# Kernel optimization log

Hardware: AMD Instinct MI355X
Metric: run time of the kernel (lower is better)

The kernel has to match this reference:

```python
import jax, jax.numpy as jnp
import numpy as np

B, C, INNER, H, W = 32, 256, 128, 32, 32
EPS = 1e-5


def _conv1x1(x, w):
    # x: (B, Cin, H, W); w: (Cout, Cin) -> (B, Cout, H, W)
    return jnp.einsum('bchw,oc->bohw', x, w)


def _attend(q, k, v):
    # q,k: (B, D, H, W); v: (B, C, H, W)
    b, d, h, w = q.shape
    n = h * w
    qf = q.reshape(b, d, n).transpose(0, 2, 1)            # (B, N, D)
    kf = k.reshape(b, d, n).transpose(0, 2, 1)            # (B, N, D)
    vf = v.reshape(b, v.shape[1], n).transpose(0, 2, 1)   # (B, N, C)
    scale = 1.0 / jnp.sqrt(jnp.asarray(d, qf.dtype))
    attn = jax.nn.softmax(jnp.einsum('bnd,bmd->bnm', qf, kf) * scale, axis=-1)
    of = jnp.einsum('bnm,bmc->bnc', attn, vf)             # (B, N, C)
    return of.transpose(0, 2, 1).reshape(b, -1, h, w)


def _layernorm(x, w, b):
    # Normalize over (C, H, W) jointly; affine params broadcast from (C,1,1).
    mu = jnp.mean(x, axis=(1, 2, 3), keepdims=True)
    var = jnp.mean(jnp.square(x - mu), axis=(1, 2, 3), keepdims=True)
    return (x - mu) * jax.lax.rsqrt(var + EPS) * w[None] + b[None]


def setup_inputs() -> dict:
    key = jax.random.key(0)
    ks = jax.random.split(key, 10)
    s = 0.02
    return {
        'fs': jax.random.normal(ks[0], (B, C, H, W), jnp.float32),
        'fi': jax.random.normal(ks[1], (B, C, H, W), jnp.float32),
        'qs_w': jax.random.normal(ks[2], (INNER, C), jnp.float32) * s,
        'ks_w': jax.random.normal(ks[3], (INNER, C), jnp.float32) * s,
        'vs_w': jax.random.normal(ks[4], (C, C), jnp.float32) * s,
        'qi_w': jax.random.normal(ks[5], (INNER, C), jnp.float32) * s,
        'ki_w': jax.random.normal(ks[6], (INNER, C), jnp.float32) * s,
        'vi_w': jax.random.normal(ks[7], (C, C), jnp.float32) * s,
        'fuse_w': jax.random.normal(ks[8], (C, 2 * C), jnp.float32) * s,
        'fuse_b': jnp.zeros((C,), jnp.float32),
        'ln_s_w': jnp.ones((C, 1, 1), jnp.float32),
        'ln_s_b': jnp.zeros((C, 1, 1), jnp.float32),
        'ln_i_w': jnp.ones((C, 1, 1), jnp.float32),
        'ln_i_b': jnp.zeros((C, 1, 1), jnp.float32),
    }


def reference(fs, fi, qs_w, ks_w, vs_w, qi_w, ki_w, vi_w,
              fuse_w, fuse_b, ln_s_w, ln_s_b, ln_i_w, ln_i_b):
    # sketch queries attend over image keys/values
    s2i = _attend(_conv1x1(fs, qs_w), _conv1x1(fi, ki_w), _conv1x1(fi, vi_w))
    # image queries attend over sketch keys/values
    i2s = _attend(_conv1x1(fi, qi_w), _conv1x1(fs, ks_w), _conv1x1(fs, vs_w))

    def fuse(x):
        return jax.nn.relu(_conv1x1(x, fuse_w) + fuse_b[None, :, None, None])

    fs_out = _layernorm(fuse(jnp.concatenate([fs, i2s], axis=1)) + fs, ln_s_w, ln_s_b)
    fi_out = _layernorm(fuse(jnp.concatenate([fi, s2i], axis=1)) + fi, ln_i_w, ln_i_b)
    return (fs_out, fi_out)
```

## Files before the change

### kernel.cpp

```cpp
#include <hip/hip_runtime.h>

typedef unsigned short u16;
typedef unsigned int   u32;

#define B_   32
#define C_   256
#define N_   1024
#define CN_  (C_*N_)
#define EPS_ 1e-5f

typedef __attribute__((ext_vector_type(8))) short  short8;
typedef __attribute__((ext_vector_type(4))) float  f32x4;

__device__ __forceinline__ float b2f(u16 u){
  union { u32 u; float f; } c; c.u = ((u32)u) << 16; return c.f;
}
__device__ __forceinline__ u16 f2b(float f){
  union { float f; u32 u; } c; c.f = f;
  u32 u = c.u;
  return (u16)((u + 0x7FFFu + ((u >> 16) & 1u)) >> 16);
}

struct F4v { float v[4]; };

__device__ __forceinline__ F4v ld4g(const void* p, long i, int bf){
  F4v r;
  if (bf){
    ushort4 u = *(const ushort4*)((const u16*)p + i);
    r.v[0]=b2f(u.x); r.v[1]=b2f(u.y); r.v[2]=b2f(u.z); r.v[3]=b2f(u.w);
  } else {
    float4 f = *(const float4*)((const float*)p + i);
    r.v[0]=f.x; r.v[1]=f.y; r.v[2]=f.z; r.v[3]=f.w;
  }
  return r;
}
__device__ __forceinline__ float ld1g(const void* p, long i, int bf){
  return bf ? b2f(((const u16*)p)[i]) : ((const float*)p)[i];
}
__device__ __forceinline__ void st1g(void* p, long i, float v, int bf){
  if (bf) ((u16*)p)[i] = f2b(v); else ((float*)p)[i] = v;
}
__device__ __forceinline__ void st4g(void* p, long i, const float* v, int bf){
  if (bf){
    ushort4 u;
    u.x=f2b(v[0]); u.y=f2b(v[1]); u.z=f2b(v[2]); u.w=f2b(v[3]);
    *(ushort4*)((u16*)p + i) = u;
  } else {
    *(float4*)((float*)p + i) = make_float4(v[0],v[1],v[2],v[3]);
  }
}
__device__ __forceinline__ int sniff_bf(const void* lnw){
  return (*(const u32*)lnw == 0x3F803F80u) ? 1 : 0;
}

__global__ __launch_bounds__(256) void k_prep_w(
    const void* qs, const void* ks, const void* vs,
    const void* qi, const void* ki, const void* vi,
    const void* fw, const void* lnw,
    u16* __restrict__ Wcat, u16* __restrict__ fuseWb, float* __restrict__ stats)
{
  const int bf = sniff_bf(lnw);
  if (blockIdx.x == 0 && threadIdx.x < 128) stats[threadIdx.x] = 0.0f;
  const long idx = ((long)blockIdx.x*256 + threadIdx.x) * 4;
  if (idx < 262144){
    const int side = (int)(idx >> 17);
    const int rem  = (int)(idx & 131071);
    const int row  = rem >> 8, col = rem & 255;
    const void* src; int r2;
    if (row < 128)      { src = side ? qi : qs; r2 = row; }
    else if (row < 256) { src = side ? ki : ks; r2 = row - 128; }
    else                { src = side ? vi : vs; r2 = row - 256; }
    F4v v = ld4g(src, (long)r2*256 + col, bf);
    ushort4 u; u.x=f2b(v.v[0]); u.y=f2b(v.v[1]); u.z=f2b(v.v[2]); u.w=f2b(v.v[3]);
    *(ushort4*)&Wcat[idx] = u;
  } else {
    const long j = idx - 262144;
    F4v v = ld4g(fw, j, bf);
    ushort4 u; u.x=f2b(v.v[0]); u.y=f2b(v.v[1]); u.z=f2b(v.v[2]); u.w=f2b(v.v[3]);
    *(ushort4*)&fuseWb[j] = u;
  }
}

__global__ __launch_bounds__(256) void k_prep_t(
    const void* fs, const void* fi, const void* lnw, u16* __restrict__ Ft)
{
  const int bf = sniff_bf(lnw);
  const int nt = blockIdx.x, ct = blockIdx.y, bs = blockIdx.z;
  const int b = bs >> 1, side = bs & 1;
  const void* F = side ? fi : fs;
  const int t = threadIdx.x;
  __shared__ u16 T[64][72];
  const int c0 = ct << 6, n0 = nt << 6;
  const int nc = (t & 15) << 2, cl = t >> 4;
  #pragma unroll
  for (int p = 0; p < 4; p++){
    const int c = cl + (p << 4);
    F4v v = ld4g(F, ((long)b*C_ + c0 + c)*N_ + n0 + nc, bf);
    T[nc  ][c] = f2b(v.v[0]);
    T[nc+1][c] = f2b(v.v[1]);
    T[nc+2][c] = f2b(v.v[2]);
    T[nc+3][c] = f2b(v.v[3]);
  }
  __syncthreads();
  const int nl = t >> 2, cc = (t & 3) << 4;
  float4 x0 = *(const float4*)&T[nl][cc];
  float4 x1 = *(const float4*)&T[nl][cc + 8];
  u16* dst = Ft + ((long)bs << 18) + (long)(n0 + nl)*256 + c0 + cc;
  *(float4*)dst = x0;
  *(float4*)(dst + 8) = x1;
}

__global__ __launch_bounds__(256) void k_proj(
    const u16* __restrict__ Wcat, const u16* __restrict__ Ft,
    u16* __restrict__ QKp, u16* __restrict__ Vp)
{
  const int nt = blockIdx.x;
  const int ot = blockIdx.y;
  const int bs = blockIdx.z;
  const int side = bs & 1;
  const int t = threadIdx.x;
  const int wv = t >> 6, li = t & 15, qd = (t >> 4) & 3;
  const int o0 = (ot << 7) + (wv << 5);
  const int n0 = nt << 7;

  const u16* ap = Wcat + ((long)side*512 + o0 + li)*256 + qd*8;
  const u16* bp = Ft + ((long)bs << 18) + (long)(n0 + li)*256 + qd*8;

  const f32x4 z4 = {0.f,0.f,0.f,0.f};
  f32x4 acc[2][8];
  #pragma unroll
  for (int i = 0; i < 2; i++)
    #pragma unroll
    for (int j = 0; j < 8; j++) acc[i][j] = z4;

  for (int ks = 0; ks < 8; ks++){
    const int ko = ks*32;
    short8 a0 = *(const short8*)(ap + ko);
    short8 a1 = *(const short8*)(ap + 16*256 + ko);
    short8 bfr[8];
    #pragma unroll
    for (int j = 0; j < 8; j++) bfr[j] = *(const short8*)(bp + (long)j*16*256 + ko);
    #pragma unroll
    for (int j = 0; j < 8; j++){
      acc[0][j] = __builtin_amdgcn_mfma_f32_16x16x32_bf16(a0, bfr[j], acc[0][j], 0, 0, 0);
      acc[1][j] = __builtin_amdgcn_mfma_f32_16x16x32_bf16(a1, bfr[j], acc[1][j], 0, 0, 0);
    }
  }

  if (o0 < 256){
    u16* base = QKp + ((long)bs << 18);
    #pragma unroll
    for (int mi = 0; mi < 2; mi++){
      const int ocol = o0 + mi*16 + qd*4;
      #pragma unroll
      for (int j = 0; j < 8; j++){
        const int n = n0 + j*16 + li;
        ushort4 u;
        u.x = f2b(acc[mi][j][0]); u.y = f2b(acc[mi][j][1]);
        u.z = f2b(acc[mi][j][2]); u.w = f2b(acc[mi][j][3]);
        *(ushort4*)&base[(long)n*256 + ocol] = u;
      }
    }
  } else {
    u16* base = Vp + ((long)bs << 18);
    #pragma unroll
    for (int mi = 0; mi < 2; mi++){
      #pragma unroll
      for (int j = 0; j < 8; j++){
        const int n = n0 + j*16 + li;
        #pragma unroll
        for (int r = 0; r < 4; r++){
          const int c = o0 - 256 + mi*16 + qd*4 + r;
          base[(long)c*N_ + n] = f2b(acc[mi][j][r]);
        }
      }
    }
  }
}

__global__ __launch_bounds__(256) void k_attn(
    const u16* __restrict__ QKp, const u16* __restrict__ Vp, u16* __restrict__ AOt)
{
  const int nt = blockIdx.x;
  const int tt = blockIdx.y;
  const int b  = blockIdx.z;
  const int qside = 1 - tt, kvside = tt;
  const u16* Qb = QKp + (((long)(b*2+qside)) << 18);
  const u16* Kb = QKp + (((long)(b*2+kvside)) << 18) + 128;
  const u16* Vb = Vp  + (((long)(b*2+kvside)) << 18);

  const int t  = threadIdx.x;
  const int wv = t >> 6;
  const int li = t & 15;
  const int qd = (t >> 4) & 3;
  const int n0 = nt << 6;
  const int qb = wv << 4;
  const int cb = wv << 6;

  __shared__ __align__(16) u16 Pt[64][72];
  __shared__ float alphaS[64];
  __shared__ float lS[64];

  short8 qf[4];
  {
    const u16* qrow = Qb + (long)(n0 + qb + li)*256 + qd*8;
    #pragma unroll
    for (int kk = 0; kk < 4; kk++) qf[kk] = *(const short8*)(qrow + kk*32);
  }

  const f32x4 z4 = {0.f, 0.f, 0.f, 0.f};
  f32x4 accO[4][4];
  #pragma unroll
  for (int i = 0; i < 4; i++)
    #pragma unroll
    for (int j = 0; j < 4; j++) accO[i][j] = z4;
  float mst[4], lst[4];
  #pragma unroll
  for (int r = 0; r < 4; r++){ mst[r] = -1e30f; lst[r] = 0.0f; }
  const float scale = 0.088388347648318447f;

  for (int mt = 0; mt < 16; mt++){
    const int m0 = mt << 6;
    f32x4 sf[4];
    #pragma unroll
    for (int j = 0; j < 4; j++) sf[j] = z4;
    {
      const u16* krow = Kb + (long)(m0 + li)*256 + qd*8;
      #pragma unroll
      for (int j4 = 0; j4 < 4; j4++){
        #pragma unroll
        for (int kk = 0; kk < 4; kk++){
          short8 kf = *(const short8*)(krow + (long)j4*16*256 + kk*32);
          sf[j4] = __builtin_amdgcn_mfma_f32_16x16x32_bf16(qf[kk], kf, sf[j4], 0, 0, 0);
        }
      }
    }
    float al4[4];
    #pragma unroll
    for (int r = 0; r < 4; r++){
      float v0 = sf[0][r]*scale, v1 = sf[1][r]*scale;
      float v2 = sf[2][r]*scale, v3 = sf[3][r]*scale;
      float mx = fmaxf(fmaxf(v0,v1), fmaxf(v2,v3));
      mx = fmaxf(mx, __shfl_xor(mx, 1, 64));
      mx = fmaxf(mx, __shfl_xor(mx, 2, 64));
      mx = fmaxf(mx, __shfl_xor(mx, 4, 64));
      mx = fmaxf(mx, __shfl_xor(mx, 8, 64));
      float mn = fmaxf(mst[r], mx);
      float a  = __expf(mst[r] - mn);
      float p0 = __expf(v0 - mn), p1 = __expf(v1 - mn);
      float p2 = __expf(v2 - mn), p3 = __expf(v3 - mn);
      const int q = qb + (qd<<2) + r;
      Pt[q][     li] = f2b(p0);
      Pt[q][16 + li] = f2b(p1);
      Pt[q][32 + li] = f2b(p2);
      Pt[q][48 + li] = f2b(p3);
      float sm = p0 + p1 + p2 + p3;
      sm += __shfl_xor(sm, 1, 64);
      sm += __shfl_xor(sm, 2, 64);
      sm += __shfl_xor(sm, 4, 64);
      sm += __shfl_xor(sm, 8, 64);
      lst[r] = lst[r]*a + sm;
      mst[r] = mn;
      al4[r] = a;
    }
    if (li == 0){
      #pragma unroll
      for (int r = 0; r < 4; r++) alphaS[qb + (qd<<2) + r] = al4[r];
    }
    __syncthreads();
    {
      float aq[4];
      #pragma unroll
      for (int j4 = 0; j4 < 4; j4++) aq[j4] = alphaS[(j4<<4) + li];
      #pragma unroll
      for (int i4 = 0; i4 < 4; i4++)
        #pragma unroll
        for (int j4 = 0; j4 < 4; j4++){
          accO[i4][j4][0] *= aq[j4]; accO[i4][j4][1] *= aq[j4];
          accO[i4][j4][2] *= aq[j4]; accO[i4][j4][3] *= aq[j4];
        }
      short8 va[4][2];
      const u16* vrow = Vb + (long)(cb + li)*N_ + m0 + qd*8;
      #pragma unroll
      for (int i4 = 0; i4 < 4; i4++){
        va[i4][0] = *(const short8*)(vrow + (long)i4*16*N_);
        va[i4][1] = *(const short8*)(vrow + (long)i4*16*N_ + 32);
      }
      #pragma unroll
      for (int j4 = 0; j4 < 4; j4++){
        short8 pb0 = *(const short8*)&Pt[(j4<<4) + li][qd*8];
        short8 pb1 = *(const short8*)&Pt[(j4<<4) + li][qd*8 + 32];
        #pragma unroll
        for (int i4 = 0; i4 < 4; i4++){
          accO[i4][j4] = __builtin_amdgcn_mfma_f32_16x16x32_bf16(va[i4][0], pb0, accO[i4][j4], 0, 0, 0);
          accO[i4][j4] = __builtin_amdgcn_mfma_f32_16x16x32_bf16(va[i4][1], pb1, accO[i4][j4], 0, 0, 0);
        }
      }
    }
    __syncthreads();
  }
  if (li == 0){
    #pragma unroll
    for (int r = 0; r < 4; r++) lS[qb + (qd<<2) + r] = lst[r];
  }
  __syncthreads();
  float linv[4];
  #pragma unroll
  for (int j4 = 0; j4 < 4; j4++) linv[j4] = 1.0f / lS[(j4<<4) + li];
  u16* aob = AOt + (((long)(b*2+tt)) << 18);
  #pragma unroll
  for (int i4 = 0; i4 < 4; i4++){
    #pragma unroll
    for (int j4 = 0; j4 < 4; j4++){
      const int n = n0 + (j4<<4) + li;
      ushort4 u;
      u.x = f2b(accO[i4][j4][0] * linv[j4]);
      u.y = f2b(accO[i4][j4][1] * linv[j4]);
      u.z = f2b(accO[i4][j4][2] * linv[j4]);
      u.w = f2b(accO[i4][j4][3] * linv[j4]);
      *(ushort4*)&aob[(long)n*256 + cb + (i4<<4) + (qd<<2)] = u;
    }
  }
}

__global__ __launch_bounds__(256) void k_fuse(
    const void* fs, const void* fi, const u16* __restrict__ fuseWb,
    const void* fbias, const u16* __restrict__ Ft, const u16* __restrict__ AOt,
    void* out, float* __restrict__ stats, const void* lnw)
{
  const int bf = sniff_bf(lnw);
  const int nt = blockIdx.x;
  const int ot = blockIdx.y;
  const int bw = blockIdx.z;
  const int b = bw >> 1, w = bw & 1;
  const void* F = w ? fi : fs;
  const int t = threadIdx.x;
  const int wv = t >> 6, li = t & 15, qd = (t >> 4) & 3;
  const int o0 = (ot << 7) + (wv << 5);
  const int n0 = nt << 7;

  const u16* ap  = fuseWb + (long)(o0 + li)*512 + qd*8;
  const u16* bp1 = Ft  + ((long)bw << 18) + (long)(n0 + li)*256 + qd*8;
  const u16* bp2 = AOt + ((long)bw << 18) + (long)(n0 + li)*256 + qd*8;

  const f32x4 z4 = {0.f,0.f,0.f,0.f};
  f32x4 acc[2][8];
  #pragma unroll
  for (int i = 0; i < 2; i++)
    #pragma unroll
    for (int j = 0; j < 8; j++) acc[i][j] = z4;

  for (int ks = 0; ks < 16; ks++){
    const u16* bp = (ks < 8) ? (bp1 + ks*32) : (bp2 + (ks-8)*32);
    const int ko = ks*32;
    short8 a0 = *(const short8*)(ap + ko);
    short8 a1 = *(const short8*)(ap + 16*512 + ko);
    short8 bfr[8];
    #pragma unroll
    for (int j = 0; j < 8; j++) bfr[j] = *(const short8*)(bp + (long)j*16*256);
    #pragma unroll
    for (int j = 0; j < 8; j++){
      acc[0][j] = __builtin_amdgcn_mfma_f32_16x16x32_bf16(a0, bfr[j], acc[0][j], 0, 0, 0);
      acc[1][j] = __builtin_amdgcn_mfma_f32_16x16x32_bf16(a1, bfr[j], acc[1][j], 0, 0, 0);
    }
  }

  __shared__ float rbuf[8];
  float s1 = 0.0f, s2 = 0.0f;
  #pragma unroll
  for (int mi = 0; mi < 2; mi++){
    float biasv[4];
    #pragma unroll
    for (int r = 0; r < 4; r++) biasv[r] = ld1g(fbias, o0 + mi*16 + qd*4 + r, bf);
    #pragma unroll
    for (int j = 0; j < 8; j++){
      const int n = n0 + j*16 + li;
      #pragma unroll
      for (int r = 0; r < 4; r++){
        const int o = o0 + mi*16 + qd*4 + r;
        const float res = ld1g(F, ((long)b*C_ + o)*N_ + n, bf);
        float y = acc[mi][j][r] + biasv[r];
        y = y > 0.0f ? y : 0.0f;
        y += res;
        s1 += y; s2 += y*y;
        st1g(out, ((long)w*B_ + b)*CN_ + (long)o*N_ + n, y, bf);
      }
    }
  }
  #pragma unroll
  for (int off = 32; off > 0; off >>= 1){
    s1 += __shfl_down(s1, off, 64);
    s2 += __shfl_down(s2, off, 64);
  }
  const int lane = t & 63;
  if (lane == 0){ rbuf[wv*2] = s1; rbuf[wv*2+1] = s2; }
  __syncthreads();
  if (t == 0){
    atomicAdd(&stats[bw*2  ], rbuf[0]+rbuf[2]+rbuf[4]+rbuf[6]);
    atomicAdd(&stats[bw*2+1], rbuf[1]+rbuf[3]+rbuf[5]+rbuf[7]);
  }
}

__global__ __launch_bounds__(256) void k_ln(
    void* out, const float* __restrict__ stats,
    const void* lsw, const void* lsb, const void* liw, const void* lib)
{
  const int bf = sniff_bf(lsw);
  const long g = ((long)blockIdx.x*256 + threadIdx.x) * 4;
  const long half = (long)B_*CN_;
  const int w = (g >= half) ? 1 : 0;
  const long rem = g - (long)w*half;
  const int b  = (int)(rem >> 18);
  const int cn = (int)(rem & (CN_-1));
  const int c  = cn >> 10;
  const float s1v = stats[(b*2+w)*2], s2v = stats[(b*2+w)*2+1];
  const float inv = 1.0f / (float)CN_;
  const float mean = s1v * inv;
  const float var  = s2v * inv - mean*mean;
  const float rstd = rsqrtf(var + EPS_);
  const float lw = ld1g(w ? liw : lsw, c, bf);
  const float lb = ld1g(w ? lib : lsb, c, bf);
  F4v x = ld4g(out, g, bf);
  float vv[4];
  #pragma unroll
  for (int j = 0; j < 4; j++) vv[j] = (x.v[j] - mean)*rstd*lw + lb;
  st4g(out, g, vv, bf);
}

extern "C" void kernel_launch(void* const* d_in, const int* in_sizes, int n_in,
                              void* d_out, int out_size, void* d_ws, size_t ws_size,
                              hipStream_t stream)
{
  const void* fs     = d_in[0];
  const void* fi     = d_in[1];
  const void* qs_w   = d_in[2];
  const void* ks_w   = d_in[3];
  const void* vs_w   = d_in[4];
  const void* qi_w   = d_in[5];
  const void* ki_w   = d_in[6];
  const void* vi_w   = d_in[7];
  const void* fuse_w = d_in[8];
  const void* fuse_b = d_in[9];
  const void* ln_s_w = d_in[10];
  const void* ln_s_b = d_in[11];
  const void* ln_i_w = d_in[12];
  const void* ln_i_b = d_in[13];

  char* ws = (char*)d_ws;
  float* stats  = (float*)ws;
  u16*   Wcat   = (u16*)(ws + 4096);
  u16*   fuseWb = (u16*)(ws + 4096 + 524288);
  u16*   Ft     = (u16*)(ws + (1u<<20));
  u16*   QKp    = (u16*)(ws + (1u<<20) + (1u<<25));
  u16*   Vp     = (u16*)(ws + (1u<<20) + 2u*(1u<<25));
  u16*   AOt    = (u16*)(ws + (1u<<20) + 3u*(1u<<25));

  k_prep_w<<<dim3(384), dim3(256), 0, stream>>>(
      qs_w, ks_w, vs_w, qi_w, ki_w, vi_w, fuse_w, ln_s_w, Wcat, fuseWb, stats);
  k_prep_t<<<dim3(16,4,64), dim3(256), 0, stream>>>(fs, fi, ln_s_w, Ft);
  k_proj<<<dim3(8,4,64), dim3(256), 0, stream>>>(Wcat, Ft, QKp, Vp);
  k_attn<<<dim3(16,2,32), dim3(256), 0, stream>>>(QKp, Vp, AOt);
  k_fuse<<<dim3(8,2,64), dim3(256), 0, stream>>>(
      fs, fi, fuseWb, fuse_b, Ft, AOt, d_out, stats, ln_s_w);
  k_ln<<<dim3(16384), dim3(256), 0, stream>>>(
      d_out, stats, ln_s_w, ln_s_b, ln_i_w, ln_i_b);
}
```

Measured before the change: 559.3 us.

## Double-buffer K fragments in registers and prefetch V early in attention kernel

The attention loop now loads the next K tile into a second register buffer while the current tile's QK MFMAs run, and issues V loads before the score computation so their latency overlaps softmax work. The grid is flattened to 1D with (batch, side) pairs as the fastest-varying index, which changes block scheduling and L2 locality for K/V. Launch bounds now request two blocks per SIMD-group, which caps register use even though the prefetch buffers add register pressure. Spilling is the main risk.

```diff
diff --git a/kernel.cpp b/kernel.cpp
--- a/kernel.cpp
+++ b/kernel.cpp
@@ -178,12 +178,103 @@
   }
 }
 
-__global__ __launch_bounds__(256) void k_attn(
+#define ATTN_STEP(MT, KCUR, KNXT)                                              \
+{                                                                              \
+  const int m0s = (MT) << 6;                                                   \
+                     \
+  short8 va[8];                                                                \
+  {                                                                            \
+    const u16* vrow = Vb + (long)(cb + li)*N_ + m0s + qd*8;                    \
+    _Pragma("unroll")                                                          \
+    for (int i4 = 0; i4 < 4; i4++){                                            \
+      va[i4*2  ] = *(const short8*)(vrow + (long)i4*16*N_);                    \
+      va[i4*2+1] = *(const short8*)(vrow + (long)i4*16*N_ + 32);               \
+    }                                                                          \
+  }                                                                            \
+                                        \
+  f32x4 sf[4];                                                                 \
+  sf[0]=z4; sf[1]=z4; sf[2]=z4; sf[3]=z4;                                      \
+  _Pragma("unroll")                                                            \
+  for (int j4 = 0; j4 < 4; j4++)                                               \
+    _Pragma("unroll")                                                          \
+    for (int kk = 0; kk < 4; kk++)                                             \
+      sf[j4] = __builtin_amdgcn_mfma_f32_16x16x32_bf16(qf[kk], KCUR[j4*4+kk], sf[j4], 0, 0, 0); \
+     \
+  if ((MT) + 1 < 16){                                                          \
+    const u16* krow = Kb + (long)((((MT)+1) << 6) + li)*256 + qd*8;            \
+    _Pragma("unroll")                                                          \
+    for (int j4 = 0; j4 < 4; j4++)                                             \
+      _Pragma("unroll")                                                        \
+      for (int kk = 0; kk < 4; kk++)                                           \
+        KNXT[j4*4+kk] = *(const short8*)(krow + (long)j4*16*256 + kk*32);      \
+  }                                                                            \
+                                \
+  float al4[4];                                                                \
+  _Pragma("unroll")                                                            \
+  for (int r = 0; r < 4; r++){                                                 \
+    float v0 = sf[0][r]*scale, v1 = sf[1][r]*scale;                            \
+    float v2 = sf[2][r]*scale, v3 = sf[3][r]*scale;                            \
+    float mx = fmaxf(fmaxf(v0,v1), fmaxf(v2,v3));                              \
+    mx = fmaxf(mx, __shfl_xor(mx, 1, 64));                                     \
+    mx = fmaxf(mx, __shfl_xor(mx, 2, 64));                                     \
+    mx = fmaxf(mx, __shfl_xor(mx, 4, 64));                                     \
+    mx = fmaxf(mx, __shfl_xor(mx, 8, 64));                                     \
+    float mn = fmaxf(mst[r], mx);                                              \
+    float a  = __expf(mst[r] - mn);                                            \
+    float p0 = __expf(v0 - mn), p1 = __expf(v1 - mn);                          \
+    float p2 = __expf(v2 - mn), p3 = __expf(v3 - mn);                          \
+    const int q = qb + (qd<<2) + r;                                            \
+    Pt[q][     li] = f2b(p0);                                                  \
+    Pt[q][16 + li] = f2b(p1);                                                  \
+    Pt[q][32 + li] = f2b(p2);                                                  \
+    Pt[q][48 + li] = f2b(p3);                                                  \
+    float sm = p0 + p1 + p2 + p3;                                              \
+    sm += __shfl_xor(sm, 1, 64);                                               \
+    sm += __shfl_xor(sm, 2, 64);                                               \
+    sm += __shfl_xor(sm, 4, 64);                                               \
+    sm += __shfl_xor(sm, 8, 64);                                               \
+    lst[r] = lst[r]*a + sm;                                                    \
+    mst[r] = mn;                                                               \
+    al4[r] = a;                                                                \
+  }                                                                            \
+  if (li == 0){                                                                \
+    _Pragma("unroll")                                                          \
+    for (int r = 0; r < 4; r++) alphaS[qb + (qd<<2) + r] = al4[r];             \
+  }                                                                            \
+  __syncthreads();                                                             \
+                                                  \
+  {                                                                            \
+    float aq[4];                                                               \
+    _Pragma("unroll")                                                          \
+    for (int j4 = 0; j4 < 4; j4++) aq[j4] = alphaS[(j4<<4) + li];              \
+    _Pragma("unroll")                                                          \
+    for (int i4 = 0; i4 < 4; i4++)                                             \
+      _Pragma("unroll")                                                        \
+      for (int j4 = 0; j4 < 4; j4++){                                          \
+        accO[i4][j4][0] *= aq[j4]; accO[i4][j4][1] *= aq[j4];                  \
+        accO[i4][j4][2] *= aq[j4]; accO[i4][j4][3] *= aq[j4];                  \
+      }                                                                        \
+    _Pragma("unroll")                                                          \
+    for (int j4 = 0; j4 < 4; j4++){                                            \
+      short8 pb0 = *(const short8*)&Pt[(j4<<4) + li][qd*8];                    \
+      short8 pb1 = *(const short8*)&Pt[(j4<<4) + li][qd*8 + 32];               \
+      _Pragma("unroll")                                                        \
+      for (int i4 = 0; i4 < 4; i4++){                                          \
+        accO[i4][j4] = __builtin_amdgcn_mfma_f32_16x16x32_bf16(va[i4*2  ], pb0, accO[i4][j4], 0, 0, 0); \
+        accO[i4][j4] = __builtin_amdgcn_mfma_f32_16x16x32_bf16(va[i4*2+1], pb1, accO[i4][j4], 0, 0, 0); \
+      }                                                                        \
+    }                                                                          \
+  }                                                                            \
+  __syncthreads();                                                             \
+}
+
+__global__ __launch_bounds__(256, 2) void k_attn(
     const u16* __restrict__ QKp, const u16* __restrict__ Vp, u16* __restrict__ AOt)
 {
-  const int nt = blockIdx.x;
-  const int tt = blockIdx.y;
-  const int b  = blockIdx.z;
+  const int id   = blockIdx.x;
+  const int pair = id & 63;
+  const int nt   = id >> 6;
+  const int b  = pair >> 1, tt = pair & 1;
   const int qside = 1 - tt, kvside = tt;
   const u16* Qb = QKp + (((long)(b*2+qside)) << 18);
   const u16* Kb = QKp + (((long)(b*2+kvside)) << 18) + 128;
@@ -219,86 +310,21 @@
   for (int r = 0; r < 4; r++){ mst[r] = -1e30f; lst[r] = 0.0f; }
   const float scale = 0.088388347648318447f;
 
-  for (int mt = 0; mt < 16; mt++){
-    const int m0 = mt << 6;
-    f32x4 sf[4];
-    #pragma unroll
-    for (int j = 0; j < 4; j++) sf[j] = z4;
-    {
-      const u16* krow = Kb + (long)(m0 + li)*256 + qd*8;
+  short8 kfA[16], kfB[16];
+  {
+    const u16* krow = Kb + (long)li*256 + qd*8;
+    #pragma unroll
+    for (int j4 = 0; j4 < 4; j4++)
       #pragma unroll
-      for (int j4 = 0; j4 < 4; j4++){
-        #pragma unroll
-        for (int kk = 0; kk < 4; kk++){
-          short8 kf = *(const short8*)(krow + (long)j4*16*256 + kk*32);
-          sf[j4] = __builtin_amdgcn_mfma_f32_16x16x32_bf16(qf[kk], kf, sf[j4], 0, 0, 0);
-        }
-      }
-    }
-    float al4[4];
-    #pragma unroll
-    for (int r = 0; r < 4; r++){
-      float v0 = sf[0][r]*scale, v1 = sf[1][r]*scale;
-      float v2 = sf[2][r]*scale, v3 = sf[3][r]*scale;
-      float mx = fmaxf(fmaxf(v0,v1), fmaxf(v2,v3));
-      mx = fmaxf(mx, __shfl_xor(mx, 1, 64));
-      mx = fmaxf(mx, __shfl_xor(mx, 2, 64));
-      mx = fmaxf(mx, __shfl_xor(mx, 4, 64));
-      mx = fmaxf(mx, __shfl_xor(mx, 8, 64));
-      float mn = fmaxf(mst[r], mx);
-      float a  = __expf(mst[r] - mn);
-      float p0 = __expf(v0 - mn), p1 = __expf(v1 - mn);
-      float p2 = __expf(v2 - mn), p3 = __expf(v3 - mn);
-      const int q = qb + (qd<<2) + r;
-      Pt[q][     li] = f2b(p0);
-      Pt[q][16 + li] = f2b(p1);
-      Pt[q][32 + li] = f2b(p2);
-      Pt[q][48 + li] = f2b(p3);
-      float sm = p0 + p1 + p2 + p3;
-      sm += __shfl_xor(sm, 1, 64);
-      sm += __shfl_xor(sm, 2, 64);
-      sm += __shfl_xor(sm, 4, 64);
-      sm += __shfl_xor(sm, 8, 64);
-      lst[r] = lst[r]*a + sm;
-      mst[r] = mn;
-      al4[r] = a;
-    }
-    if (li == 0){
-      #pragma unroll
-      for (int r = 0; r < 4; r++) alphaS[qb + (qd<<2) + r] = al4[r];
-    }
-    __syncthreads();
-    {
-      float aq[4];
-      #pragma unroll
-      for (int j4 = 0; j4 < 4; j4++) aq[j4] = alphaS[(j4<<4) + li];
-      #pragma unroll
-      for (int i4 = 0; i4 < 4; i4++)
-        #pragma unroll
-        for (int j4 = 0; j4 < 4; j4++){
-          accO[i4][j4][0] *= aq[j4]; accO[i4][j4][1] *= aq[j4];
-          accO[i4][j4][2] *= aq[j4]; accO[i4][j4][3] *= aq[j4];
-        }
-      short8 va[4][2];
-      const u16* vrow = Vb + (long)(cb + li)*N_ + m0 + qd*8;
-      #pragma unroll
-      for (int i4 = 0; i4 < 4; i4++){
-        va[i4][0] = *(const short8*)(vrow + (long)i4*16*N_);
-        va[i4][1] = *(const short8*)(vrow + (long)i4*16*N_ + 32);
-      }
-      #pragma unroll
-      for (int j4 = 0; j4 < 4; j4++){
-        short8 pb0 = *(const short8*)&Pt[(j4<<4) + li][qd*8];
-        short8 pb1 = *(const short8*)&Pt[(j4<<4) + li][qd*8 + 32];
-        #pragma unroll
-        for (int i4 = 0; i4 < 4; i4++){
-          accO[i4][j4] = __builtin_amdgcn_mfma_f32_16x16x32_bf16(va[i4][0], pb0, accO[i4][j4], 0, 0, 0);
-          accO[i4][j4] = __builtin_amdgcn_mfma_f32_16x16x32_bf16(va[i4][1], pb1, accO[i4][j4], 0, 0, 0);
-        }
-      }
-    }
-    __syncthreads();
-  }
+      for (int kk = 0; kk < 4; kk++)
+        kfA[j4*4+kk] = *(const short8*)(krow + (long)j4*16*256 + kk*32);
+  }
+
+  for (int mt2 = 0; mt2 < 16; mt2 += 2){
+    ATTN_STEP(mt2,     kfA, kfB)
+    ATTN_STEP(mt2 + 1, kfB, kfA)
+  }
+
   if (li == 0){
     #pragma unroll
     for (int r = 0; r < 4; r++) lS[qb + (qd<<2) + r] = lst[r];
@@ -459,7 +485,7 @@
       qs_w, ks_w, vs_w, qi_w, ki_w, vi_w, fuse_w, ln_s_w, Wcat, fuseWb, stats);
   k_prep_t<<<dim3(16,4,64), dim3(256), 0, stream>>>(fs, fi, ln_s_w, Ft);
   k_proj<<<dim3(8,4,64), dim3(256), 0, stream>>>(Wcat, Ft, QKp, Vp);
-  k_attn<<<dim3(16,2,32), dim3(256), 0, stream>>>(QKp, Vp, AOt);
+  k_attn<<<dim3(1024), dim3(256), 0, stream>>>(QKp, Vp, AOt);
   k_fuse<<<dim3(8,2,64), dim3(256), 0, stream>>>(
       fs, fi, fuseWb, fuse_b, Ft, AOt, d_out, stats, ln_s_w);
   k_ln<<<dim3(16384), dim3(256), 0, stream>>>(
```

Result: slower. 667.8 us (+19.4%).
